# Kernel optimization log

Hardware: AMD Instinct MI355X
Metric: run time of the kernel (lower is better)

The kernel has to match this reference:

```python
import jax, jax.numpy as jnp
import numpy as np

B, N, C, H = 8, 4096, 1024, 16
D = C // H  # head_dim = 64
EPS = 1e-12

def _l2norm(x):
    # F.normalize(x, p=2, dim=-1): x / max(||x||_2, eps)
    n = jnp.sqrt(jnp.sum(x * x, axis=-1, keepdims=True))
    return x / jnp.maximum(n, EPS)

def setup_inputs() -> dict:
    key = jax.random.key(0)
    ks = jax.random.split(key, 5)
    return {
        "x": jax.random.normal(ks[0], (B, N, C), dtype=jnp.float32),
        "qkv_w": jax.random.normal(ks[1], (C, 3 * C), dtype=jnp.float32) * 0.02,
        "qkv_b": jax.random.normal(ks[2], (3 * C,), dtype=jnp.float32) * 0.02,
        "proj_w": jax.random.normal(ks[3], (C, C), dtype=jnp.float32) * 0.02,
        "proj_b": jax.random.normal(ks[4], (C,), dtype=jnp.float32) * 0.02,
    }

def reference(x, qkv_w, qkv_b, proj_w, proj_b):
    b, n, c = x.shape
    qkv = (x @ qkv_w + qkv_b).reshape(b, n, 3, H, D)
    qkv = jnp.transpose(qkv, (2, 0, 3, 1, 4))  # [3,B,H,N,D]
    q, k, v = qkv[0], qkv[1], qkv[2]
    q = _l2norm(q)
    k = _l2norm(k)
    kv = jnp.einsum('bhnd,bhne->bhde', k, v)   # small [B,H,D,D] state
    out = jnp.einsum('bhnd,bhde->bhne', q, kv)  # [B,H,N,D]
    out = jnp.transpose(out, (0, 2, 1, 3)).reshape(b, n, c)
    return out @ proj_w + proj_b
```

## Files before the change

kernel.cpp:

```cpp
#include <hip/hip_runtime.h>
#include <stdint.h>

#define B_ 8
#define N_ 4096
#define C_ 1024
#define H_ 16
#define M_ (B_*N_)
#define BH_ (B_*H_)

typedef unsigned short u16;
typedef unsigned int   u32;
typedef __bf16 bf16x8 __attribute__((ext_vector_type(8)));
typedef float  f32x4  __attribute__((ext_vector_type(4)));

__device__ __forceinline__ u16 f2bf(float f) {
  union { float f; u32 u; } x; x.f = f;
  u32 r = x.u + 0x7fffu + ((x.u >> 16) & 1u);
  return (u16)(r >> 16);
}
__device__ __forceinline__ float bf2f(u16 b) {
  union { u32 u; float f; } x; x.u = ((u32)b) << 16;
  return x.f;
}
__device__ __forceinline__ void gload16(const void* g, void* l) {
  __builtin_amdgcn_global_load_lds(
      (const __attribute__((address_space(1))) void*)g,
      (__attribute__((address_space(3))) void*)l,
      16, 0, 0);
}
__device__ __forceinline__ void unpack8(uint4 r, float* f) {
  const u32 w[4] = {r.x, r.y, r.z, r.w};
#pragma unroll
  for (int i = 0; i < 4; ++i) {
    f[2*i]   = bf2f((u16)(w[i] & 0xffffu));
    f[2*i+1] = bf2f((u16)(w[i] >> 16));
  }
}
__device__ __forceinline__ uint4 pack8(const float* f) {
  uint4 r; u32* w = (u32*)&r;
#pragma unroll
  for (int i = 0; i < 4; ++i)
    w[i] = (u32)f2bf(f[2*i]) | ((u32)f2bf(f[2*i+1]) << 16);
  return r;
}
__device__ __forceinline__ bf16x8 packbf8(const float* f) {
  uint4 p = pack8(f);
  return *reinterpret_cast<bf16x8*>(&p);
}

__global__ void cast_f32_bf16(const float* __restrict__ in, u16* __restrict__ out, int n4) {
  int i = blockIdx.x * blockDim.x + threadIdx.x;
  const int stride = gridDim.x * blockDim.x;
  for (; i < n4; i += stride) {
    float4 v = reinterpret_cast<const float4*>(in)[i];
    u32 lo = (u32)f2bf(v.x) | ((u32)f2bf(v.y) << 16);
    u32 hi = (u32)f2bf(v.z) | ((u32)f2bf(v.w) << 16);
    uint2 o; o.x = lo; o.y = hi;
    reinterpret_cast<uint2*>(out)[i] = o;
  }
}

__global__ void transpose_cast(const float* __restrict__ in, u16* __restrict__ out,
                               int R, int Cc) {
  __shared__ float t[32][33];
  const int bx = blockIdx.x * 32;
  const int by = blockIdx.y * 32;
  const int tx = threadIdx.x & 31;
  const int ty = threadIdx.x >> 5;
#pragma unroll
  for (int j = 0; j < 4; ++j) {
    const int r = by + ty + j * 8;
    t[ty + j * 8][tx] = in[(size_t)r * Cc + bx + tx];
  }
  __syncthreads();
#pragma unroll
  for (int j = 0; j < 4; ++j) {
    const int c = bx + ty + j * 8;
    out[(size_t)c * R + by + tx] = f2bf(t[tx][ty + j * 8]);
  }
}

template <int NC, bool OUT_BF16>
__global__ __launch_bounds__(512) void gemm256(const u16* __restrict__ A,
                                               const u16* __restrict__ Bt,
                                               const float* __restrict__ bias,
                                               void* __restrict__ outp,
                                               int K, int cpx) {
  __shared__ __align__(16) u16 As[2][256][64];
  __shared__ __align__(16) u16 Bs[2][256][64];
  const int tid  = threadIdx.x;
  const int lane = tid & 63;
  const int w    = tid >> 6;
  const int wm   = (w >> 2) & 1;
  const int wn   = w & 3;
  const int l15  = lane & 15;
  const int lk   = lane >> 4;

  const int bid = blockIdx.x;
  const int wg  = (bid & 7) * cpx + (bid >> 3);
  const size_t brow = (size_t)(wg & 127) * 256;
  const size_t bcol = (size_t)(wg >> 7) * 256;

  const int KT = K >> 6;
  f32x4 acc[2][2][4][2] = {};

  auto stage = [&](const u16* __restrict__ src, size_t rowbase, int kt,
                   u16* lds_tile, int h) {
#pragma unroll
    for (int is = 0; is < 2; ++is) {
      const int lin   = is * 8192 + tid * 16;
      const int row   = lin >> 7;
      const int chunk = ((lin >> 4) & 7) ^ (row & 7);
      gload16(src + (rowbase + (size_t)(h * 128 + row)) * K + kt * 64 + chunk * 8,
              (char*)lds_tile + h * 16384 + lin);
    }
  };
  auto fragA = [&](const u16* tb, int mh, int mf, int kc) -> bf16x8 {
    const int row   = mh * 128 + wm * 64 + mf * 16 + l15;
    const int chunk = ((kc << 2) | lk) ^ (row & 7);
    return *reinterpret_cast<const bf16x8*>((const char*)tb + row * 128 + chunk * 16);
  };
  auto fragB = [&](const u16* tb, int nh, int nf, int kc) -> bf16x8 {
    const int row   = nh * 128 + wn * 32 + nf * 16 + l15;
    const int chunk = ((kc << 2) | lk) ^ (row & 7);
    return *reinterpret_cast<const bf16x8*>((const char*)tb + row * 128 + chunk * 16);
  };

#define MFMA_Q(AF, BF, MH, NH) do {                                            \
    __builtin_amdgcn_s_barrier();                                              \
    __builtin_amdgcn_s_setprio(1);                                             \
    _Pragma("unroll") for (int mf = 0; mf < 4; ++mf)                           \
      _Pragma("unroll") for (int nf = 0; nf < 2; ++nf)                         \
        _Pragma("unroll") for (int kc = 0; kc < 2; ++kc)                       \
          acc[MH][NH][mf][nf] = __builtin_amdgcn_mfma_f32_16x16x32_bf16(       \
              AF[mf][kc], BF[nf][kc], acc[MH][NH][mf][nf], 0, 0, 0);           \
    __builtin_amdgcn_s_setprio(0);                                             \
    __builtin_amdgcn_s_barrier();                                              \
  } while (0)

  stage(A,  brow, 0, &As[0][0][0], 0);
  stage(Bt, bcol, 0, &Bs[0][0][0], 0);
  stage(A,  brow, 0, &As[0][0][0], 1);
  stage(Bt, bcol, 0, &Bs[0][0][0], 1);
  stage(A,  brow, 1, &As[1][0][0], 0);
  stage(Bt, bcol, 1, &Bs[1][0][0], 0);
  asm volatile("s_waitcnt vmcnt(4)" ::: "memory");
  __builtin_amdgcn_s_barrier();

  for (int t = 0; t < KT; ++t) {
    const u16* curA = &As[t & 1][0][0];
    const u16* curB = &Bs[t & 1][0][0];
    u16* nA  = &As[(t + 1) & 1][0][0];
    u16* nB  = &Bs[(t + 1) & 1][0][0];
    u16* n2A = &As[t & 1][0][0];
    u16* n2B = &Bs[t & 1][0][0];
    const bool s1 = (t + 1) < KT;
    const bool s2 = (t + 2) < KT;

    bf16x8 afA[4][2], afB[4][2], bf0[2][2], bf1[2][2];

#pragma unroll
    for (int mf = 0; mf < 4; ++mf)
#pragma unroll
      for (int kc = 0; kc < 2; ++kc) afA[mf][kc] = fragA(curA, 0, mf, kc);
#pragma unroll
    for (int nf = 0; nf < 2; ++nf)
#pragma unroll
      for (int kc = 0; kc < 2; ++kc) bf0[nf][kc] = fragB(curB, 0, nf, kc);
    if (s1) stage(A, brow, t + 1, nA, 1);
    MFMA_Q(afA, bf0, 0, 0);

#pragma unroll
    for (int nf = 0; nf < 2; ++nf)
#pragma unroll
      for (int kc = 0; kc < 2; ++kc) bf1[nf][kc] = fragB(curB, 1, nf, kc);
    if (s1) stage(Bt, bcol, t + 1, nB, 1);
    MFMA_Q(afA, bf1, 0, 1);

#pragma unroll
    for (int mf = 0; mf < 4; ++mf)
#pragma unroll
      for (int kc = 0; kc < 2; ++kc) afB[mf][kc] = fragA(curA, 1, mf, kc);
    if (s2) stage(A, brow, t + 2, n2A, 0);
    MFMA_Q(afB, bf1, 1, 1);

    if (s2) {
      stage(Bt, bcol, t + 2, n2B, 0);
      asm volatile("s_waitcnt vmcnt(4)" ::: "memory");
    } else {
      asm volatile("s_waitcnt vmcnt(0)" ::: "memory");
    }
    MFMA_Q(afB, bf0, 1, 0);
  }
#undef MFMA_Q

#pragma unroll
  for (int mh = 0; mh < 2; ++mh)
#pragma unroll
  for (int nh = 0; nh < 2; ++nh)
#pragma unroll
  for (int mf = 0; mf < 4; ++mf)
#pragma unroll
  for (int nf = 0; nf < 2; ++nf) {
    const size_t col = bcol + nh * 128 + wn * 32 + nf * 16 + l15;
    const float bv = bias[col];
    const size_t row0 = brow + mh * 128 + wm * 64 + mf * 16 + lk * 4;
#pragma unroll
    for (int r = 0; r < 4; ++r) {
      const float v = acc[mh][nh][mf][nf][r] + bv;
      if constexpr (OUT_BF16)
        ((u16*)outp)[(row0 + r) * NC + col] = f2bf(v);
      else
        ((float*)outp)[(row0 + r) * NC + col] = v;
    }
  }
}

__global__ void qsc_kernel(const u16* __restrict__ qkv, float* __restrict__ qsc) {
  const int t = threadIdx.x;
  const size_t p = (size_t)blockIdx.x * 32 + (t >> 3);
  const int c8 = t & 7;
  const size_t row = p >> 4;
  const int h = (int)(p & 15);
  uint4 raw = *reinterpret_cast<const uint4*>(qkv + row * 3072 + h * 64 + c8 * 8);
  float f[8]; unpack8(raw, f);
  float ss = 0.f;
#pragma unroll
  for (int j = 0; j < 8; ++j) ss += f[j] * f[j];
  ss += __shfl_xor(ss, 1); ss += __shfl_xor(ss, 2); ss += __shfl_xor(ss, 4);
  if (c8 == 0) qsc[p] = 1.f / fmaxf(sqrtf(ss), 1e-12f);
}

__global__ __launch_bounds__(256) void kv_fused(const u16* __restrict__ qkv,
                                                float* __restrict__ part) {
  const int bh = blockIdx.x, sp = blockIdx.y;
  const int b = bh >> 4, h = bh & 15;
  const int tid  = threadIdx.x;
  const int lane = tid & 63;
  const int w    = tid >> 6;
  const int wm   = w >> 1, wn = w & 1;
  const int l15  = lane & 15;
  const int lk   = lane >> 4;

  __shared__ float Ks[64 * 65];
  __shared__ float Vs[64 * 65];

  f32x4 acc[2][2] = {};
  const size_t nbase = (size_t)b * N_ + (size_t)sp * 512;

  for (int ch = 0; ch < 8; ++ch) {
    __syncthreads();
#pragma unroll
    for (int it = 0; it < 2; ++it) {
      const int idx = it * 256 + tid;
      const int r = idx >> 3, c8 = idx & 7;
      const size_t rowoff = (nbase + (size_t)(ch * 64 + r)) * 3072 + h * 64 + c8 * 8;
      uint4 kraw = *reinterpret_cast<const uint4*>(qkv + rowoff + 1024);
      float kf[8]; unpack8(kraw, kf);
      float ss = 0.f;
#pragma unroll
      for (int j = 0; j < 8; ++j) ss += kf[j] * kf[j];
      ss += __shfl_xor(ss, 1); ss += __shfl_xor(ss, 2); ss += __shfl_xor(ss, 4);
      const float sc = 1.f / fmaxf(sqrtf(ss), 1e-12f);
#pragma unroll
      for (int j = 0; j < 8; ++j) Ks[r * 65 + c8 * 8 + j] = kf[j] * sc;
      uint4 vraw = *reinterpret_cast<const uint4*>(qkv + rowoff + 2048);
      float vf[8]; unpack8(vraw, vf);
#pragma unroll
      for (int j = 0; j < 8; ++j) Vs[r * 65 + c8 * 8 + j] = vf[j];
    }
    __syncthreads();

    bf16x8 fa[2][2], fb[2][2];
#pragma unroll
    for (int mf = 0; mf < 2; ++mf)
#pragma unroll
      for (int kc = 0; kc < 2; ++kc) {
        const int e = wm * 32 + mf * 16 + l15;
        float tmp[8];
#pragma unroll
        for (int j = 0; j < 8; ++j) tmp[j] = Vs[(kc * 32 + lk * 8 + j) * 65 + e];
        fa[mf][kc] = packbf8(tmp);
      }
#pragma unroll
    for (int nf = 0; nf < 2; ++nf)
#pragma unroll
      for (int kc = 0; kc < 2; ++kc) {
        const int d = wn * 32 + nf * 16 + l15;
        float tmp[8];
#pragma unroll
        for (int j = 0; j < 8; ++j) tmp[j] = Ks[(kc * 32 + lk * 8 + j) * 65 + d];
        fb[nf][kc] = packbf8(tmp);
      }
#pragma unroll
    for (int mf = 0; mf < 2; ++mf)
#pragma unroll
      for (int nf = 0; nf < 2; ++nf)
#pragma unroll
        for (int kc = 0; kc < 2; ++kc)
          acc[mf][nf] = __builtin_amdgcn_mfma_f32_16x16x32_bf16(
              fa[mf][kc], fb[nf][kc], acc[mf][nf], 0, 0, 0);
  }

  float* base = part + ((size_t)sp * BH_ + bh) * 4096;
#pragma unroll
  for (int mf = 0; mf < 2; ++mf)
#pragma unroll
    for (int nf = 0; nf < 2; ++nf)
#pragma unroll
      for (int r = 0; r < 4; ++r) {
        const int e = wm * 32 + mf * 16 + lk * 4 + r;
        const int d = wn * 32 + nf * 16 + l15;
        base[e * 64 + d] = acc[mf][nf][r];
      }
}

__global__ void kv_reduce8(const float* __restrict__ part, u16* __restrict__ kvT) {
  const int i4 = (blockIdx.x * 256 + threadIdx.x) * 4;
  float4 s = *reinterpret_cast<const float4*>(part + i4);
#pragma unroll
  for (int sp = 1; sp < 8; ++sp) {
    float4 p = *reinterpret_cast<const float4*>(part + (size_t)sp * 524288 + i4);
    s.x += p.x; s.y += p.y; s.z += p.z; s.w += p.w;
  }
  u32 lo = (u32)f2bf(s.x) | ((u32)f2bf(s.y) << 16);
  u32 hi = (u32)f2bf(s.z) | ((u32)f2bf(s.w) << 16);
  uint2 o; o.x = lo; o.y = hi;
  *reinterpret_cast<uint2*>(kvT + i4) = o;
}

__global__ void attn_gemm(const u16* __restrict__ qkv, const u16* __restrict__ kvT,
                          const float* __restrict__ qsc, u16* __restrict__ attn) {
  const int bh = blockIdx.x, nt = blockIdx.y;
  const int b = bh >> 4, h = bh & 15;
  const int n0 = nt * 128;
  __shared__ __align__(16) u16 Qs[128 * 64];
  __shared__ __align__(16) u16 Ks[64 * 64];
  const int tid  = threadIdx.x;
  const int lane = tid & 63;
  const int wm   = tid >> 6;
  const int l15  = lane & 15;
  const int lk   = lane >> 4;

#pragma unroll
  for (int is = 0; is < 4; ++is) {
    const int lin   = is * 4096 + tid * 16;
    const int row   = lin >> 7;
    const int chunk = ((lin >> 4) & 7) ^ (row & 7);
    gload16(qkv + ((size_t)(b * N_ + n0 + row)) * 3072 + h * 64 + chunk * 8,
            (char*)Qs + lin);
  }
#pragma unroll
  for (int is = 0; is < 2; ++is) {
    const int lin   = is * 4096 + tid * 16;
    const int row   = lin >> 7;
    const int chunk = ((lin >> 4) & 7) ^ (row & 7);
    gload16(kvT + (size_t)bh * 4096 + row * 64 + chunk * 8, (char*)Ks + lin);
  }
  __syncthreads();

  bf16x8 fq[2][2], fk[4][2];
#pragma unroll
  for (int mf = 0; mf < 2; ++mf)
#pragma unroll
    for (int kc = 0; kc < 2; ++kc) {
      const int row = wm * 32 + mf * 16 + l15;
      const int chunk = ((kc << 2) | lk) ^ (row & 7);
      fq[mf][kc] = *reinterpret_cast<const bf16x8*>((const char*)Qs + row * 128 + chunk * 16);
    }
#pragma unroll
  for (int nf = 0; nf < 4; ++nf)
#pragma unroll
    for (int kc = 0; kc < 2; ++kc) {
      const int row = nf * 16 + l15;
      const int chunk = ((kc << 2) | lk) ^ (row & 7);
      fk[nf][kc] = *reinterpret_cast<const bf16x8*>((const char*)Ks + row * 128 + chunk * 16);
    }
  f32x4 acc[2][4] = {};
#pragma unroll
  for (int mf = 0; mf < 2; ++mf)
#pragma unroll
    for (int nf = 0; nf < 4; ++nf)
#pragma unroll
      for (int kc = 0; kc < 2; ++kc)
        acc[mf][nf] = __builtin_amdgcn_mfma_f32_16x16x32_bf16(
            fq[mf][kc], fk[nf][kc], acc[mf][nf], 0, 0, 0);

#pragma unroll
  for (int mf = 0; mf < 2; ++mf)
#pragma unroll
    for (int r = 0; r < 4; ++r) {
      const size_t row = (size_t)(b * N_ + n0 + wm * 32 + mf * 16 + lk * 4 + r);
      const float sc = qsc[row * 16 + h];
#pragma unroll
      for (int nf = 0; nf < 4; ++nf)
        attn[row * 1024 + h * 64 + nf * 16 + l15] = f2bf(acc[mf][nf][r] * sc);
    }
}

#define WS_XB     0ull
#define WS_QKV    67108864ull
#define WS_VT     268435456ull
#define WS_WQKV   335544320ull
#define WS_WPROJ  341835776ull
#define WS_QSC    343932928ull
#define WS_KVT    360710144ull

extern "C" void kernel_launch(void* const* d_in, const int* in_sizes, int n_in,
                              void* d_out, int out_size, void* d_ws, size_t ws_size,
                              hipStream_t stream) {
  const float* x      = (const float*)d_in[0];
  const float* qkv_w  = (const float*)d_in[1];
  const float* qkv_b  = (const float*)d_in[2];
  const float* proj_w = (const float*)d_in[3];
  const float* proj_b = (const float*)d_in[4];

  char* ws = (char*)d_ws;
  u16*   xb      = (u16*)(ws + WS_XB);
  u16*   qkv     = (u16*)(ws + WS_QKV);
  float* part    = (float*)(ws + WS_VT);
  u16*   attn    = (u16*)(ws + WS_VT);
  u16*   wqkv_t  = (u16*)(ws + WS_WQKV);
  u16*   wproj_t = (u16*)(ws + WS_WPROJ);
  float* qsc     = (float*)(ws + WS_QSC);
  u16*   kvT     = (u16*)(ws + WS_KVT);

  cast_f32_bf16<<<2048, 256, 0, stream>>>(x, xb, (M_ * C_) / 4);
  transpose_cast<<<dim3(96, 32), 256, 0, stream>>>(qkv_w, wqkv_t, 1024, 3072);
  transpose_cast<<<dim3(32, 32), 256, 0, stream>>>(proj_w, wproj_t, 1024, 1024);
  gemm256<3072, true><<<1536, 512, 0, stream>>>(xb, wqkv_t, qkv_b, qkv, 1024, 192);
  qsc_kernel<<<16384, 256, 0, stream>>>(qkv, qsc);
  kv_fused<<<dim3(128, 8), 256, 0, stream>>>(qkv, part);
  kv_reduce8<<<512, 256, 0, stream>>>(part, kvT);
  attn_gemm<<<dim3(128, 32), 256, 0, stream>>>(qkv, kvT, qsc, attn);
  gemm256<1024, false><<<512, 512, 0, stream>>>(attn, wproj_t, proj_b, d_out, 1024, 64);
}
```

Before: 452.8 us.

## Software-pipeline LDS fragment reads with MFMA quads in 256x256 GEMM

Restructures the GEMM main loop to unroll by two k-tiles and prefetch the next LDS fragments (A/B halves) before each MFMA quad. Explicit lgkmcnt waits let ds_reads for the following quad overlap the current quad's MFMAs, instead of loading fragments just before use. This hides LDS latency behind tensor math at the cost of more live fragment registers and a trickier barrier and waitcnt schedule. The last iteration reads fragments past the final tile, and there is a risk of race or register-pressure issues.

```diff
diff --git a/kernel.cpp b/kernel.cpp
--- a/kernel.cpp
+++ b/kernel.cpp
@@ -47,6 +47,10 @@
   uint4 p = pack8(f);
   return *reinterpret_cast<bf16x8*>(&p);
 }
+
+#define BAR       __builtin_amdgcn_s_barrier()
+#define LGKM(N)   asm volatile("s_waitcnt lgkmcnt(" #N ")" ::: "memory")
+#define VMCNT(N)  asm volatile("s_waitcnt vmcnt(" #N ")" ::: "memory")
 
 __global__ void cast_f32_bf16(const float* __restrict__ in, u16* __restrict__ out, int n4) {
   int i = blockIdx.x * blockDim.x + threadIdx.x;
@@ -86,8 +90,8 @@
                                                const float* __restrict__ bias,
                                                void* __restrict__ outp,
                                                int K, int cpx) {
-  __shared__ __align__(16) u16 As[2][256][64];
-  __shared__ __align__(16) u16 Bs[2][256][64];
+  __shared__ __align__(16) u16 As[2][256 * 64];
+  __shared__ __align__(16) u16 Bs[2][256 * 64];
   const int tid  = threadIdx.x;
   const int lane = tid & 63;
   const int w    = tid >> 6;
@@ -101,7 +105,7 @@
   const size_t brow = (size_t)(wg & 127) * 256;
   const size_t bcol = (size_t)(wg >> 7) * 256;
 
-  const int KT = K >> 6;
+  const int KTn = K >> 6;
   f32x4 acc[2][2][4][2] = {};
 
   auto stage = [&](const u16* __restrict__ src, size_t rowbase, int kt,
@@ -115,84 +119,106 @@
               (char*)lds_tile + h * 16384 + lin);
     }
   };
-  auto fragA = [&](const u16* tb, int mh, int mf, int kc) -> bf16x8 {
-    const int row   = mh * 128 + wm * 64 + mf * 16 + l15;
-    const int chunk = ((kc << 2) | lk) ^ (row & 7);
-    return *reinterpret_cast<const bf16x8*>((const char*)tb + row * 128 + chunk * 16);
+  auto readA = [&](bf16x8 (&d)[4][2], const u16* tb, int mh) {
+#pragma unroll
+    for (int mf = 0; mf < 4; ++mf)
+#pragma unroll
+      for (int kc = 0; kc < 2; ++kc) {
+        const int row   = mh * 128 + wm * 64 + mf * 16 + l15;
+        const int chunk = ((kc << 2) | lk) ^ (row & 7);
+        d[mf][kc] = *reinterpret_cast<const bf16x8*>((const char*)tb + row * 128 + chunk * 16);
+      }
   };
-  auto fragB = [&](const u16* tb, int nh, int nf, int kc) -> bf16x8 {
-    const int row   = nh * 128 + wn * 32 + nf * 16 + l15;
-    const int chunk = ((kc << 2) | lk) ^ (row & 7);
-    return *reinterpret_cast<const bf16x8*>((const char*)tb + row * 128 + chunk * 16);
+  auto readB = [&](bf16x8 (&d)[2][2], const u16* tb, int nh) {
+#pragma unroll
+    for (int nf = 0; nf < 2; ++nf)
+#pragma unroll
+      for (int kc = 0; kc < 2; ++kc) {
+        const int row   = nh * 128 + wn * 32 + nf * 16 + l15;
+        const int chunk = ((kc << 2) | lk) ^ (row & 7);
+        d[nf][kc] = *reinterpret_cast<const bf16x8*>((const char*)tb + row * 128 + chunk * 16);
+      }
   };
-
-#define MFMA_Q(AF, BF, MH, NH) do {                                            \
-    __builtin_amdgcn_s_barrier();                                              \
-    __builtin_amdgcn_s_setprio(1);                                             \
-    _Pragma("unroll") for (int mf = 0; mf < 4; ++mf)                           \
-      _Pragma("unroll") for (int nf = 0; nf < 2; ++nf)                         \
-        _Pragma("unroll") for (int kc = 0; kc < 2; ++kc)                       \
-          acc[MH][NH][mf][nf] = __builtin_amdgcn_mfma_f32_16x16x32_bf16(       \
-              AF[mf][kc], BF[nf][kc], acc[MH][NH][mf][nf], 0, 0, 0);           \
-    __builtin_amdgcn_s_setprio(0);                                             \
-    __builtin_amdgcn_s_barrier();                                              \
-  } while (0)
-
-  stage(A,  brow, 0, &As[0][0][0], 0);
-  stage(Bt, bcol, 0, &Bs[0][0][0], 0);
-  stage(A,  brow, 0, &As[0][0][0], 1);
-  stage(Bt, bcol, 0, &Bs[0][0][0], 1);
-  stage(A,  brow, 1, &As[1][0][0], 0);
-  stage(Bt, bcol, 1, &Bs[1][0][0], 0);
-  asm volatile("s_waitcnt vmcnt(4)" ::: "memory");
-  __builtin_amdgcn_s_barrier();
-
-  for (int t = 0; t < KT; ++t) {
-    const u16* curA = &As[t & 1][0][0];
-    const u16* curB = &Bs[t & 1][0][0];
-    u16* nA  = &As[(t + 1) & 1][0][0];
-    u16* nB  = &Bs[(t + 1) & 1][0][0];
-    u16* n2A = &As[t & 1][0][0];
-    u16* n2B = &Bs[t & 1][0][0];
-    const bool s1 = (t + 1) < KT;
-    const bool s2 = (t + 2) < KT;
-
-    bf16x8 afA[4][2], afB[4][2], bf0[2][2], bf1[2][2];
-
-#pragma unroll
-    for (int mf = 0; mf < 4; ++mf)
-#pragma unroll
-      for (int kc = 0; kc < 2; ++kc) afA[mf][kc] = fragA(curA, 0, mf, kc);
-#pragma unroll
-    for (int nf = 0; nf < 2; ++nf)
-#pragma unroll
-      for (int kc = 0; kc < 2; ++kc) bf0[nf][kc] = fragB(curB, 0, nf, kc);
-    if (s1) stage(A, brow, t + 1, nA, 1);
-    MFMA_Q(afA, bf0, 0, 0);
-
-#pragma unroll
-    for (int nf = 0; nf < 2; ++nf)
-#pragma unroll
-      for (int kc = 0; kc < 2; ++kc) bf1[nf][kc] = fragB(curB, 1, nf, kc);
-    if (s1) stage(Bt, bcol, t + 1, nB, 1);
-    MFMA_Q(afA, bf1, 0, 1);
-
-#pragma unroll
-    for (int mf = 0; mf < 4; ++mf)
-#pragma unroll
-      for (int kc = 0; kc < 2; ++kc) afB[mf][kc] = fragA(curA, 1, mf, kc);
-    if (s2) stage(A, brow, t + 2, n2A, 0);
-    MFMA_Q(afB, bf1, 1, 1);
-
-    if (s2) {
-      stage(Bt, bcol, t + 2, n2B, 0);
-      asm volatile("s_waitcnt vmcnt(4)" ::: "memory");
-    } else {
-      asm volatile("s_waitcnt vmcnt(0)" ::: "memory");
-    }
-    MFMA_Q(afB, bf0, 1, 0);
-  }
-#undef MFMA_Q
+  auto quad = [&](bf16x8 (&af)[4][2], bf16x8 (&bf)[2][2], f32x4 (&ac)[4][2]) {
+    __builtin_amdgcn_s_setprio(1);
+#pragma unroll
+    for (int kc = 0; kc < 2; ++kc)
+#pragma unroll
+      for (int mf = 0; mf < 4; ++mf)
+#pragma unroll
+        for (int nf = 0; nf < 2; ++nf)
+          ac[mf][nf] = __builtin_amdgcn_mfma_f32_16x16x32_bf16(
+              af[mf][kc], bf[nf][kc], ac[mf][nf], 0, 0, 0);
+    __builtin_amdgcn_s_setprio(0);
+  };
+
+  bf16x8 a0[4][2], a1[4][2], b1[2][2], b0e[2][2], b0o[2][2];
+
+  stage(A,  brow, 0, As[0], 0);
+  stage(Bt, bcol, 0, Bs[0], 0);
+  stage(A,  brow, 0, As[0], 1);
+  stage(Bt, bcol, 0, Bs[0], 1);
+  stage(A,  brow, 1, As[1], 0);
+  stage(Bt, bcol, 1, Bs[1], 0);
+  VMCNT(4);
+  BAR;
+  readA(a0, As[0], 0);
+  readB(b0e, Bs[0], 0);
+
+  for (int tt = 0; tt < KTn; tt += 2) {
+    const bool s2 = (tt + 2) < KTn;
+    const bool s3 = (tt + 3) < KTn;
+
+    readB(b1, Bs[0], 1);
+    stage(A, brow, tt + 1, As[1], 1);
+    BAR; LGKM(4);
+    quad(a0, b0e, acc[0][0]);
+    BAR;
+
+    readA(a1, As[0], 1);
+    stage(Bt, bcol, tt + 1, Bs[1], 1);
+    BAR; LGKM(8);
+    quad(a0, b1, acc[0][1]);
+    BAR;
+
+    readB(b0o, Bs[1], 0);
+    if (s2) stage(A, brow, tt + 2, As[0], 0);
+    BAR; LGKM(4);
+    quad(a1, b1, acc[1][1]);
+    BAR;
+
+    readA(a0, As[1], 0);
+    if (s2) { stage(Bt, bcol, tt + 2, Bs[0], 0); VMCNT(4); }
+    else    { VMCNT(0); }
+    BAR; LGKM(8);
+    quad(a1, b0e, acc[1][0]);
+    BAR;
+
+    readB(b1, Bs[1], 1);
+    if (s2) stage(A, brow, tt + 2, As[0], 1);
+    BAR; LGKM(4);
+    quad(a0, b0o, acc[0][0]);
+    BAR;
+
+    readA(a1, As[1], 1);
+    if (s2) stage(Bt, bcol, tt + 2, Bs[0], 1);
+    BAR; LGKM(8);
+    quad(a0, b1, acc[0][1]);
+    BAR;
+
+    readB(b0e, Bs[0], 0);
+    if (s3) stage(A, brow, tt + 3, As[1], 0);
+    BAR; LGKM(4);
+    quad(a1, b1, acc[1][1]);
+    BAR;
+
+    readA(a0, As[0], 0);
+    if (s3) { stage(Bt, bcol, tt + 3, Bs[1], 0); VMCNT(4); }
+    else    { VMCNT(0); }
+    BAR; LGKM(8);
+    quad(a1, b0o, acc[1][0]);
+    BAR;
+  }
 
 #pragma unroll
   for (int mh = 0; mh < 2; ++mh)
```

Result: slower. 606.1 us (+33.9%).

## Fuse query norm into attn_gemm, retile GEMM block order, add LDS wait

Applied to the files above, without the earlier changes.

Removes the separate qsc_kernel and instead computes each query row's inverse L2 norm inside attn_gemm from the Q tile already staged in shared memory. This saves one launch plus a global read of Q and a write and read of the scale buffer, at the cost of an extra barrier and serial per-row work by half the threads. The GEMM block-to-tile mapping is also changed to group four column tiles per row tile, for better L2 reuse of weights. An explicit lgkmcnt(0) wait is added before each MFMA quarter.

```diff
diff --git a/kernel.cpp b/kernel.cpp
--- a/kernel.cpp
+++ b/kernel.cpp
@@ -98,8 +98,9 @@
 
   const int bid = blockIdx.x;
   const int wg  = (bid & 7) * cpx + (bid >> 3);
-  const size_t brow = (size_t)(wg & 127) * 256;
-  const size_t bcol = (size_t)(wg >> 7) * 256;
+  const int col = ((wg >> 9) << 2) | (wg & 3);
+  const size_t brow = (size_t)((wg >> 2) & 127) * 256;
+  const size_t bcol = (size_t)col * 256;
 
   const int KT = K >> 6;
   f32x4 acc[2][2][4][2] = {};
@@ -128,6 +129,7 @@
 
 #define MFMA_Q(AF, BF, MH, NH) do {                                            \
     __builtin_amdgcn_s_barrier();                                              \
+    asm volatile("s_waitcnt lgkmcnt(0)" ::: "memory");                         \
     __builtin_amdgcn_s_setprio(1);                                             \
     _Pragma("unroll") for (int mf = 0; mf < 4; ++mf)                           \
       _Pragma("unroll") for (int nf = 0; nf < 2; ++nf)                         \
@@ -202,33 +204,18 @@
   for (int mf = 0; mf < 4; ++mf)
 #pragma unroll
   for (int nf = 0; nf < 2; ++nf) {
-    const size_t col = bcol + nh * 128 + wn * 32 + nf * 16 + l15;
-    const float bv = bias[col];
+    const size_t ocol = bcol + nh * 128 + wn * 32 + nf * 16 + l15;
+    const float bv = bias[ocol];
     const size_t row0 = brow + mh * 128 + wm * 64 + mf * 16 + lk * 4;
 #pragma unroll
     for (int r = 0; r < 4; ++r) {
       const float v = acc[mh][nh][mf][nf][r] + bv;
       if constexpr (OUT_BF16)
-        ((u16*)outp)[(row0 + r) * NC + col] = f2bf(v);
+        ((u16*)outp)[(row0 + r) * NC + ocol] = f2bf(v);
       else
-        ((float*)outp)[(row0 + r) * NC + col] = v;
-    }
-  }
-}
-
-__global__ void qsc_kernel(const u16* __restrict__ qkv, float* __restrict__ qsc) {
-  const int t = threadIdx.x;
-  const size_t p = (size_t)blockIdx.x * 32 + (t >> 3);
-  const int c8 = t & 7;
-  const size_t row = p >> 4;
-  const int h = (int)(p & 15);
-  uint4 raw = *reinterpret_cast<const uint4*>(qkv + row * 3072 + h * 64 + c8 * 8);
-  float f[8]; unpack8(raw, f);
-  float ss = 0.f;
-#pragma unroll
-  for (int j = 0; j < 8; ++j) ss += f[j] * f[j];
-  ss += __shfl_xor(ss, 1); ss += __shfl_xor(ss, 2); ss += __shfl_xor(ss, 4);
-  if (c8 == 0) qsc[p] = 1.f / fmaxf(sqrtf(ss), 1e-12f);
+        ((float*)outp)[(row0 + r) * NC + ocol] = v;
+    }
+  }
 }
 
 __global__ __launch_bounds__(256) void kv_fused(const u16* __restrict__ qkv,
@@ -330,12 +317,13 @@
 }
 
 __global__ void attn_gemm(const u16* __restrict__ qkv, const u16* __restrict__ kvT,
-                          const float* __restrict__ qsc, u16* __restrict__ attn) {
+                          u16* __restrict__ attn) {
   const int bh = blockIdx.x, nt = blockIdx.y;
   const int b = bh >> 4, h = bh & 15;
   const int n0 = nt * 128;
   __shared__ __align__(16) u16 Qs[128 * 64];
   __shared__ __align__(16) u16 Ks[64 * 64];
+  __shared__ float qsl[128];
   const int tid  = threadIdx.x;
   const int lane = tid & 63;
   const int wm   = tid >> 6;
@@ -359,6 +347,20 @@
   }
   __syncthreads();
 
+  if (tid < 128) {
+    float ss = 0.f;
+#pragma unroll
+    for (int c = 0; c < 8; ++c) {
+      const int ch = (c + tid) & 7;
+      uint4 raw = *reinterpret_cast<const uint4*>((const char*)Qs + tid * 128 + ch * 16);
+      float f[8]; unpack8(raw, f);
+#pragma unroll
+      for (int j = 0; j < 8; ++j) ss += f[j] * f[j];
+    }
+    qsl[tid] = 1.f / fmaxf(sqrtf(ss), 1e-12f);
+  }
+  __syncthreads();
+
   bf16x8 fq[2][2], fk[4][2];
 #pragma unroll
   for (int mf = 0; mf < 2; ++mf)
@@ -390,8 +392,9 @@
   for (int mf = 0; mf < 2; ++mf)
 #pragma unroll
     for (int r = 0; r < 4; ++r) {
-      const size_t row = (size_t)(b * N_ + n0 + wm * 32 + mf * 16 + lk * 4 + r);
-      const float sc = qsc[row * 16 + h];
+      const int rloc = wm * 32 + mf * 16 + lk * 4 + r;
+      const size_t row = (size_t)(b * N_ + n0 + rloc);
+      const float sc = qsl[rloc];
 #pragma unroll
       for (int nf = 0; nf < 4; ++nf)
         attn[row * 1024 + h * 64 + nf * 16 + l15] = f2bf(acc[mf][nf][r] * sc);
@@ -403,7 +406,6 @@
 #define WS_VT     268435456ull
 #define WS_WQKV   335544320ull
 #define WS_WPROJ  341835776ull
-#define WS_QSC    343932928ull
 #define WS_KVT    360710144ull
 
 extern "C" void kernel_launch(void* const* d_in, const int* in_sizes, int n_in,
@@ -422,16 +424,14 @@
   u16*   attn    = (u16*)(ws + WS_VT);
   u16*   wqkv_t  = (u16*)(ws + WS_WQKV);
   u16*   wproj_t = (u16*)(ws + WS_WPROJ);
-  float* qsc     = (float*)(ws + WS_QSC);
   u16*   kvT     = (u16*)(ws + WS_KVT);
 
   cast_f32_bf16<<<2048, 256, 0, stream>>>(x, xb, (M_ * C_) / 4);
   transpose_cast<<<dim3(96, 32), 256, 0, stream>>>(qkv_w, wqkv_t, 1024, 3072);
   transpose_cast<<<dim3(32, 32), 256, 0, stream>>>(proj_w, wproj_t, 1024, 1024);
   gemm256<3072, true><<<1536, 512, 0, stream>>>(xb, wqkv_t, qkv_b, qkv, 1024, 192);
-  qsc_kernel<<<16384, 256, 0, stream>>>(qkv, qsc);
   kv_fused<<<dim3(128, 8), 256, 0, stream>>>(qkv, part);
   kv_reduce8<<<512, 256, 0, stream>>>(part, kvT);
-  attn_gemm<<<dim3(128, 32), 256, 0, stream>>>(qkv, kvT, qsc, attn);
+  attn_gemm<<<dim3(128, 32), 256, 0, stream>>>(qkv, kvT, attn);
   gemm256<1024, false><<<512, 512, 0, stream>>>(attn, wproj_t, proj_b, d_out, 1024, 64);
 }
```

Result: faster. 421.6 us (-6.9%).
